# Kernel tuning notes

Hardware: AMD Instinct MI355X
Metric: run time of the kernel (lower is better)

The kernel has to match this reference:

```python
import jax, jax.numpy as jnp
import numpy as np
import math

B, N, C = 2, 2048, 1024
H, HD = 16, 64
COND_SCALE = 0.5
ROPE_THETA = 10000.0


def _layernorm(x, w, b, eps=1e-5):
    mu = jnp.mean(x, axis=-1, keepdims=True)
    var = jnp.mean(jnp.square(x - mu), axis=-1, keepdims=True)
    return (x - mu) * jax.lax.rsqrt(var + eps) * w + b


def _rope_cos_sin(n_pos, dim, dtype):
    # standard 1D RoPE: freqs over half the head dim
    inv = 1.0 / (ROPE_THETA ** (jnp.arange(0, dim, 2, dtype=jnp.float32) / dim))
    ang = jnp.arange(n_pos, dtype=jnp.float32)[:, None] * inv[None, :]  # (n_pos, dim/2)
    cos = jnp.concatenate([jnp.cos(ang), jnp.cos(ang)], axis=-1).astype(dtype)
    sin = jnp.concatenate([jnp.sin(ang), jnp.sin(ang)], axis=-1).astype(dtype)
    return cos, sin


def _apply_rope(x, cos, sin):
    # x: (B,H,N,HD); cos/sin: (N,HD)
    x1, x2 = jnp.split(x, 2, axis=-1)
    rot = jnp.concatenate([-x2, x1], axis=-1)
    return x * cos + rot * sin


def setup_inputs() -> dict:
    key = jax.random.key(0)
    ks = jax.random.split(key, 3)
    s = 1.0 / math.sqrt(C)
    return {
        "x": jax.random.normal(ks[0], (B, N, C), jnp.float32),
        "qkv_w": jax.random.normal(ks[1], (3 * C, C), jnp.float32) * s,
        "qn_w": jnp.ones((HD,), jnp.float32),
        "qn_b": jnp.zeros((HD,), jnp.float32),
        "kn_w": jnp.ones((HD,), jnp.float32),
        "kn_b": jnp.zeros((HD,), jnp.float32),
        "proj_w": jax.random.normal(ks[2], (C, C), jnp.float32) * s,
        "proj_b": jnp.zeros((C,), jnp.float32),
    }


def reference(x, qkv_w, qn_w, qn_b, kn_w, kn_b, proj_w, proj_b):
    b, n, c = x.shape
    n_in = n // 2
    qkv = (x @ qkv_w.T).reshape(b, n, 3, H, HD).transpose(2, 0, 3, 1, 4)
    q, k, v = qkv[0], qkv[1], qkv[2]  # each (B,H,N,HD)
    q = _layernorm(q, qn_w, qn_b)
    k = _layernorm(k, kn_w, kn_b)
    # conditional: rope applied per-half with positions restarting at 0,
    # i.e. cos/sin for positions [0..n_in) tiled over both halves
    cos, sin = _rope_cos_sin(n_in, HD, x.dtype)
    cos = jnp.concatenate([cos, cos], axis=0)  # (N,HD)
    sin = jnp.concatenate([sin, sin], axis=0)
    q = _apply_rope(q, cos, sin)
    k = _apply_rope(k, cos, sin)
    # attn bias: log(conditioning_scale) on cross (input<->cond) blocks
    is_input = jnp.arange(n) < n_in
    cross = is_input[:, None] != is_input[None, :]
    bias = jnp.where(cross, jnp.float32(math.log(COND_SCALE)), 0.0).astype(x.dtype)
    scale = HD ** -0.5
    scores = jnp.einsum("bhqd,bhkd->bhqk", q, k) * scale + bias
    attn = jax.nn.softmax(scores, axis=-1)
    o = jnp.einsum("bhqk,bhkd->bhqd", attn, v)
    o = o.transpose(0, 2, 1, 3).reshape(b, n, c)
    return o @ proj_w.T + proj_b
```

## Files before the change

kernel.cpp:

```cpp
#include <hip/hip_runtime.h>

#define DEVI __device__ __forceinline__

typedef __attribute__((ext_vector_type(8)))  short bh8;
typedef __attribute__((ext_vector_type(4)))  float fx4;
typedef __attribute__((ext_vector_type(16))) float fx16;

DEVI unsigned short f2b(float f){
  unsigned u = __float_as_uint(f);
  u += 0x7FFFu + ((u >> 16) & 1u);
  return (unsigned short)(u >> 16);
}
DEVI float b2f(unsigned short b){ return __uint_as_float(((unsigned)b) << 16); }

DEVI unsigned cvtpk(float a, float b){
  unsigned r;
  asm("v_cvt_pk_bf16_f32 %0, %1, %2" : "=v"(r) : "v"(a), "v"(b));
  return r;
}
DEVI float fexp2(float x){
  float r;
  asm("v_exp_f32 %0, %1" : "=v"(r) : "v"(x));
  return r;
}

typedef __attribute__((address_space(1))) const void gvoid;
typedef __attribute__((address_space(3))) void svoid;
DEVI void gload16(const void* g, void* l){
  __builtin_amdgcn_global_load_lds((gvoid*)g, (svoid*)l, 16, 0, 0);
}

union pfu { unsigned u[4]; bh8 v; };

__global__ __launch_bounds__(256) void cast3_kernel(
    const float* __restrict__ x, const float* __restrict__ w1f, const float* __restrict__ w2f,
    unsigned short* __restrict__ x16, unsigned short* __restrict__ w1, unsigned short* __restrict__ w2)
{
  int i = blockIdx.x * 256 + threadIdx.x;
  const float* src; unsigned short* dst; int off;
  if (i < 1048576)      { src = x;   dst = x16; off = i; }
  else if (i < 1835008) { src = w1f; dst = w1;  off = i - 1048576; }
  else                  { src = w2f; dst = w2;  off = i - 1835008; }
  float4 v = ((const float4*)src)[off];
  short4 r;
  r.x = (short)f2b(v.x); r.y = (short)f2b(v.y);
  r.z = (short)f2b(v.z); r.w = (short)f2b(v.w);
  ((short4*)dst)[off] = r;
}

__global__ __launch_bounds__(256) void rope_table(float* __restrict__ ct, float* __restrict__ st){
  int i = blockIdx.x * 256 + threadIdx.x;
  int pos = i >> 5, j = i & 31;
  float freq = __expf(-(float)j * 0.28782313662425576f);
  float sv, cv; sincosf((float)pos * freq, &sv, &cv);
  ct[i] = cv; st[i] = sv;
}

template<int MODE>
__global__ __launch_bounds__(256) void gemm_bt(
    const unsigned short* __restrict__ A, const unsigned short* __restrict__ B,
    unsigned short* __restrict__ Cb, float* __restrict__ Cf,
    const float* __restrict__ bias, int M, int N, int K)
{
  __shared__ char sm[49152];
  const int t = threadIdx.x, wv = t >> 6, ln = t & 63, lr = ln & 15, lg = ln >> 4;
  const int nbx = gridDim.x, nby = gridDim.y, nwg = nbx * nby;
  const int orig = blockIdx.y * nbx + blockIdx.x;
  const int w = (orig & 7) * (nwg >> 3) + (orig >> 3);
  const int bn = (w / nby) << 7, bm = (w % nby) << 7;
  const int wr = wv >> 1, wc = wv & 1;
  const fx4 fz = {0.f, 0.f, 0.f, 0.f};
  fx4 acc[4][4];
#pragma unroll
  for (int i = 0; i < 4; i++)
#pragma unroll
    for (int j = 0; j < 4; j++) acc[i][j] = fz;
  const int kiters = K >> 5;

#define GSTAGE(dst, k0) do{                                                       \
  _Pragma("unroll")                                                               \
  for (int i_ = 0; i_ < 2; i_++){                                                 \
    int c_ = i_*256 + t;                                                          \
    int row_ = c_ >> 2, col_ = (c_ & 3) << 3;                                     \
    gload16(A + (size_t)(bm + row_)*K + (k0) + col_, (dst) + i_*4096 + wv*1024);  \
    gload16(B + (size_t)(bn + row_)*K + (k0) + col_,                              \
            (dst) + 8192 + i_*4096 + wv*1024);                                    \
  } }while(0)

  char* p0 = sm; char* p1 = sm + 16384; char* p2 = sm + 32768;
  GSTAGE(p0, 0);
  GSTAGE(p1, 32);
  asm volatile("s_waitcnt vmcnt(0)" ::: "memory");
  __builtin_amdgcn_s_barrier();
  __builtin_amdgcn_sched_barrier(0);

  for (int ki = 0; ki < kiters; ++ki){
    if (ki + 2 < kiters) GSTAGE(p2, (ki + 2) << 5);
    bh8 af[4], bf[4];
#pragma unroll
    for (int mi = 0; mi < 4; mi++)
      af[mi] = *(const bh8*)(p0 + (wr*64 + mi*16 + lr)*64 + lg*16);
#pragma unroll
    for (int ni = 0; ni < 4; ni++)
      bf[ni] = *(const bh8*)(p0 + 8192 + (wc*64 + ni*16 + lr)*64 + lg*16);
    __builtin_amdgcn_s_setprio(1);
#pragma unroll
    for (int mi = 0; mi < 4; mi++)
#pragma unroll
      for (int ni = 0; ni < 4; ni++)
        acc[mi][ni] = __builtin_amdgcn_mfma_f32_16x16x32_bf16(af[mi], bf[ni], acc[mi][ni], 0, 0, 0);
    __builtin_amdgcn_s_setprio(0);
    if (ki + 2 < kiters) asm volatile("s_waitcnt vmcnt(4) lgkmcnt(0)" ::: "memory");
    else                 asm volatile("s_waitcnt vmcnt(0) lgkmcnt(0)" ::: "memory");
    __builtin_amdgcn_s_barrier();
    __builtin_amdgcn_sched_barrier(0);
    char* tmp = p0; p0 = p1; p1 = p2; p2 = tmp;
  }
#undef GSTAGE
#pragma unroll
  for (int mi = 0; mi < 4; mi++)
#pragma unroll
    for (int ni = 0; ni < 4; ni++){
      int col = bn + wc*64 + ni*16 + lr;
#pragma unroll
      for (int r = 0; r < 4; r++){
        int row = bm + wr*64 + mi*16 + lg*4 + r;
        float v = acc[mi][ni][r];
        if constexpr (MODE == 1) Cf[(size_t)row * N + col] = v + bias[col];
        else                     Cb[(size_t)row * N + col] = (short)f2b(v);
      }
    }
}

#define QSCALE 0.18033688011112042f
__global__ __launch_bounds__(256) void lnrope_kernel(
    const unsigned short* __restrict__ qkv,
    const float* __restrict__ qw, const float* __restrict__ qb,
    const float* __restrict__ kw, const float* __restrict__ kb,
    const float* __restrict__ ct, const float* __restrict__ st,
    unsigned short* __restrict__ qo, unsigned short* __restrict__ ko,
    unsigned short* __restrict__ vt)
{
  __shared__ short vl[64][66];
  const int t = threadIdx.x, wv = t >> 6, ln = t & 63;
  const int nc = blockIdx.x & 31, h = (blockIdx.x >> 5) & 15, b = blockIdx.x >> 9;
  const int j = ln & 31;
  const float gwq = qw[ln], gbq = qb[ln], gwk = kw[ln], gbk = kb[ln];
  const float sgn = (ln < 32) ? -1.0f : 1.0f;
  const size_t obase0 = ((size_t)(b*16 + h)) * 2048 * 64;
#pragma unroll 1
  for (int it = 0; it < 16; ++it){
    int nl = wv*16 + it;
    int n  = nc*64 + nl;
    size_t base = ((size_t)(b*2048 + n)) * 3072 + h*64 + ln;
    float qv = b2f(qkv[base]);
    float kv = b2f(qkv[base + 1024]);
    float vv = b2f(qkv[base + 2048]);
    float s1 = qv, s2 = qv*qv, s3 = kv, s4 = kv*kv;
#pragma unroll
    for (int off = 32; off; off >>= 1){
      s1 += __shfl_xor(s1, off); s2 += __shfl_xor(s2, off);
      s3 += __shfl_xor(s3, off); s4 += __shfl_xor(s4, off);
    }
    float mq = s1 * (1.f/64.f), mk = s3 * (1.f/64.f);
    float rq = rsqrtf(s2*(1.f/64.f) - mq*mq + 1e-5f);
    float rk = rsqrtf(s4*(1.f/64.f) - mk*mk + 1e-5f);
    float qn = (qv - mq) * rq * gwq + gbq;
    float kn = (kv - mk) * rk * gwk + gbk;
    int pos = n & 1023;
    float cv = ct[pos*32 + j], sv = st[pos*32 + j];
    float qp = __shfl_xor(qn, 32);
    float kp = __shfl_xor(kn, 32);
    size_t ob = obase0 + (size_t)n*64 + ln;
    qo[ob] = f2b((qn*cv + sgn*qp*sv) * QSCALE);
    ko[ob] = f2b(kn*cv + sgn*kp*sv);
    vl[ln][nl] = (short)f2b(vv);
  }
  __syncthreads();
  int d = t >> 2, seg = t & 3;
  size_t vb = (((size_t)(b*16 + h))*64 + d) * 2048 + nc*64 + seg*16;
#pragma unroll
  for (int u = 0; u < 4; ++u){
    short4 pk;
    pk.x = vl[d][seg*16 + u*4 + 0]; pk.y = vl[d][seg*16 + u*4 + 1];
    pk.z = vl[d][seg*16 + u*4 + 2]; pk.w = vl[d][seg*16 + u*4 + 3];
    *(short4*)&vt[vb + u*4] = pk;
  }
}

__global__ __launch_bounds__(512, 4) void attn_kernel(
    const unsigned short* __restrict__ qg, const unsigned short* __restrict__ kg,
    const unsigned short* __restrict__ vg, unsigned short* __restrict__ og)
{
  __shared__ char sm[49152];
  const int t = threadIdx.x, wv = t >> 6, ln = t & 63, lq = ln & 31, hi = ln >> 5;
  const int kvh = wv >> 2;
  const int wq  = wv & 3;
  const int swz = ((blockIdx.x & 7) << 6) | (blockIdx.x >> 3);
  const int bh = swz >> 4, q0 = (swz & 15) << 7;
  const unsigned short* kbase = kg + ((size_t)bh << 17);
  const unsigned short* vbase = vg + ((size_t)bh << 17);
  const size_t qrow = ((size_t)bh << 11) + q0 + wq*32 + lq;
  bh8 qf[4];
#pragma unroll
  for (int s2 = 0; s2 < 4; s2++) qf[s2] = *(const bh8*)&qg[qrow*64 + s2*16 + hi*8];

  fx16 o0, o1;
#pragma unroll
  for (int i = 0; i < 16; i++){ o0[i] = 0.f; o1[i] = 0.f; }
  float l_r = 0.f;
  const bool qfirst = (q0 < 1024);
  const int swsl = lq & 7;

#define STAGE(dst, kt) do{                                                        \
    int row_ = t >> 3, sl_ = (t & 7) ^ (row_ & 7);                                \
    gload16(kbase + (size_t)((kt) + row_)*64 + sl_*8, (dst) + wv*1024);           \
    gload16(vbase + (size_t)row_*2048 + (kt) + sl_*8, (dst) + 8192 + wv*1024);    \
  }while(0)

  char* p0 = sm; char* p1 = sm + 16384; char* p2 = sm + 32768;
  STAGE(p0, 0);
  STAGE(p1, 64);
  asm volatile("s_waitcnt vmcnt(0)" ::: "memory");
  __builtin_amdgcn_s_barrier();
  __builtin_amdgcn_sched_barrier(0);

  for (int tile = 0; tile < 32; ++tile){
    if (tile < 30) STAGE(p2, (tile + 2)*64);
    const char* Kc = p0;
    const char* Vc = p0 + 8192;
    const float bias2 = (qfirst != (tile < 16)) ? -1.0f : 0.0f;
    fx16 sA;
#pragma unroll
    for (int i = 0; i < 16; i++) sA[i] = bias2;
    __builtin_amdgcn_s_setprio(1);
#pragma unroll
    for (int s2 = 0; s2 < 4; s2++){
      const int slot = s2*2 + hi;
      bh8 kf = *(const bh8*)(Kc + (kvh*32 + lq)*128 + ((slot ^ swsl) << 4));
      sA = __builtin_amdgcn_mfma_f32_32x32x16_bf16(kf, qf[s2], sA, 0, 0, 0);
    }
    __builtin_amdgcn_s_setprio(0);
    bh8 vf0[2], vf1[2];
#pragma unroll
    for (int kg2 = 0; kg2 < 2; kg2++){
      const int slot = kvh*4 + kg2*2 + hi;
      vf0[kg2] = *(const bh8*)(Vc + lq*128      + ((slot ^ swsl) << 4));
      vf1[kg2] = *(const bh8*)(Vc + (32+lq)*128 + ((slot ^ swsl) << 4));
    }
    float sum = 0.f;
#pragma unroll
    for (int i = 0; i < 16; i++){
      sA[i] = fexp2(sA[i] - 16.0f);
      sum += sA[i];
    }
    sum += __shfl_xor(sum, 32);
    l_r += sum;
    bh8 pf[2];
#define MKPF(dst, sv, base) do{                                                   \
    unsigned c0 = cvtpk(sv[base+0], sv[base+1]);                                  \
    unsigned c1 = cvtpk(sv[base+2], sv[base+3]);                                  \
    unsigned c2 = cvtpk(sv[base+4], sv[base+5]);                                  \
    unsigned c3 = cvtpk(sv[base+6], sv[base+7]);                                  \
    asm volatile("v_permlane32_swap_b32 %0, %1" : "+v"(c0), "+v"(c2));            \
    asm volatile("v_permlane32_swap_b32 %0, %1" : "+v"(c1), "+v"(c3));            \
    pfu u_; u_.u[0]=c0; u_.u[1]=c1; u_.u[2]=c2; u_.u[3]=c3; dst = u_.v; }while(0)
    MKPF(pf[0], sA, 0); MKPF(pf[1], sA, 8);
#undef MKPF
    __builtin_amdgcn_s_setprio(1);
#pragma unroll
    for (int kg2 = 0; kg2 < 2; kg2++){
      o0 = __builtin_amdgcn_mfma_f32_32x32x16_bf16(vf0[kg2], pf[kg2], o0, 0, 0, 0);
      o1 = __builtin_amdgcn_mfma_f32_32x32x16_bf16(vf1[kg2], pf[kg2], o1, 0, 0, 0);
    }
    __builtin_amdgcn_s_setprio(0);
    if (tile < 30) asm volatile("s_waitcnt vmcnt(2) lgkmcnt(0)" ::: "memory");
    else           asm volatile("s_waitcnt vmcnt(0) lgkmcnt(0)" ::: "memory");
    __builtin_amdgcn_s_barrier();
    __builtin_amdgcn_sched_barrier(0);
    char* tmp = p0; p0 = p1; p1 = p2; p2 = tmp;
  }
#undef STAGE
  float* fbuf = (float*)sm;
  {
    const int base = (wq*64 + ln)*33;
    if (kvh == 1){
#pragma unroll
      for (int i = 0; i < 16; i++){ fbuf[base+i] = o0[i]; fbuf[base+16+i] = o1[i]; }
      fbuf[base+32] = l_r;
    }
  }
  __syncthreads();
  {
    const int base = (wq*64 + ln)*33;
    if (kvh == 0){
#pragma unroll
      for (int i = 0; i < 16; i++){ o0[i] += fbuf[base+i]; o1[i] += fbuf[base+16+i]; }
      l_r += fbuf[base+32];
    }
  }
  __syncthreads();
  if (kvh == 0){
    const float inv = 1.0f / l_r;
    const int ql = wq*32 + lq;
#pragma unroll
    for (int j = 0; j < 8; j++){
      int d0 = ((2*j) & 3) + 8*(j >> 1) + 4*hi;
      unsigned w0 = cvtpk(o0[2*j]*inv, o0[2*j+1]*inv);
      unsigned w1 = cvtpk(o1[2*j]*inv, o1[2*j+1]*inv);
      *(unsigned*)(sm + ql*132 + d0*2)        = w0;
      *(unsigned*)(sm + ql*132 + (32 + d0)*2) = w1;
    }
  }
  __syncthreads();
  if (t < 256){
    const int rw = t >> 1, hf = t & 1;
    const int b = bh >> 4, h = bh & 15;
    unsigned short* dst = og + ((size_t)b*2048 + q0 + rw)*1024 + h*64 + hf*32;
#pragma unroll
    for (int u = 0; u < 8; u++){
      short4 v4 = *(short4*)(sm + rw*132 + hf*64 + u*8);
      *(short4*)(dst + u*4) = v4;
    }
  }
}

extern "C" void kernel_launch(void* const* d_in, const int* in_sizes, int n_in,
                              void* d_out, int out_size, void* d_ws, size_t ws_size,
                              hipStream_t stream)
{
  const float* x      = (const float*)d_in[0];
  const float* qkv_w  = (const float*)d_in[1];
  const float* qn_w   = (const float*)d_in[2];
  const float* qn_b   = (const float*)d_in[3];
  const float* kn_w   = (const float*)d_in[4];
  const float* kn_b   = (const float*)d_in[5];
  const float* proj_w = (const float*)d_in[6];
  const float* proj_b = (const float*)d_in[7];
  float* out = (float*)d_out;

  unsigned short* x16   = (unsigned short*)d_ws;
  unsigned short* w1    = x16   + (size_t)4096*1024;
  unsigned short* w2    = w1    + (size_t)3072*1024;
  unsigned short* qkv16 = w2    + (size_t)1024*1024;
  unsigned short* q16   = qkv16 + (size_t)4096*3072;
  unsigned short* k16   = q16   + (size_t)4194304;
  unsigned short* vt16  = k16   + (size_t)4194304;
  unsigned short* o16   = qkv16;
  float* ct = (float*)x16;
  float* st = ct + 32768;

  cast3_kernel<<<8192, 256, 0, stream>>>(x, qkv_w, proj_w, x16, w1, w2);
  gemm_bt<0><<<dim3(24, 32), 256, 0, stream>>>(x16, w1, qkv16, nullptr, nullptr, 4096, 3072, 1024);
  rope_table<<<128, 256, 0, stream>>>(ct, st);
  lnrope_kernel<<<1024, 256, 0, stream>>>(qkv16, qn_w, qn_b, kn_w, kn_b, ct, st, q16, k16, vt16);
  attn_kernel<<<512, 512, 0, stream>>>(q16, k16, vt16, o16);
  gemm_bt<1><<<dim3(8, 32), 256, 0, stream>>>(o16, w2, nullptr, out, proj_b, 4096, 1024, 1024);
}
```

Before: 138.3 us.

## Add 256x256-tile 4-stage pipelined GEMM for the QKV projection

Replaces the 128x128-tile GEMM for the QKV projection with a new kernel. It uses 256x256 output tiles, 512 threads per block and a 4-deep shared-memory ring of async global-to-LDS loads with explicit vmcnt waits. The larger tiles cut global reloads of A and B and give each wave more MFMA work per LDS read. In exchange, 128KB of LDS limits the kernel to one block per CU, and the grid is only 192 blocks, which may leave compute units idle. The LDS reads are also not swizzled, so bank conflicts may occur.

```diff
diff --git a/kernel.cpp b/kernel.cpp
--- a/kernel.cpp
+++ b/kernel.cpp
@@ -54,6 +54,81 @@
   float freq = __expf(-(float)j * 0.28782313662425576f);
   float sv, cv; sincosf((float)pos * freq, &sv, &cv);
   ct[i] = cv; st[i] = sv;
+}
+
+__global__ __launch_bounds__(512, 2) void gemm256(
+    const unsigned short* __restrict__ A, const unsigned short* __restrict__ B,
+    unsigned short* __restrict__ Cb, int M, int N, int K)
+{
+  __shared__ char sm[131072];
+  const int t = threadIdx.x, wv = t >> 6, ln = t & 63, lr = ln & 15, lg = ln >> 4;
+  const int wr = wv >> 2, wc = wv & 3;
+  const int nwg = gridDim.x * gridDim.y, nby = gridDim.y;
+  const int orig = blockIdx.y * gridDim.x + blockIdx.x;
+  const int w = (orig & 7) * (nwg >> 3) + (orig >> 3);
+  const int bn = (w / nby) << 8, bm = (w % nby) << 8;
+  const fx4 fz = {0.f, 0.f, 0.f, 0.f};
+  fx4 acc[8][4];
+#pragma unroll
+  for (int i = 0; i < 8; i++)
+#pragma unroll
+    for (int j = 0; j < 4; j++) acc[i][j] = fz;
+  const int kiters = K >> 5;
+
+#define GSTAGE(buf, k0) do{                                                       \
+  char* dst_ = sm + ((buf) << 15);                                                \
+  _Pragma("unroll")                                                               \
+  for (int i_ = 0; i_ < 2; i_++){                                                 \
+    int c_ = i_*512 + t;                                                          \
+    int row_ = c_ >> 2, col_ = (c_ & 3) << 3;                                     \
+    gload16(A + (size_t)(bm + row_)*K + (k0) + col_, dst_ + i_*8192 + wv*1024);   \
+    gload16(B + (size_t)(bn + row_)*K + (k0) + col_,                              \
+            dst_ + 16384 + i_*8192 + wv*1024);                                    \
+  } }while(0)
+
+  GSTAGE(0, 0);
+  GSTAGE(1, 32);
+  GSTAGE(2, 64);
+  asm volatile("s_waitcnt vmcnt(0)" ::: "memory");
+  __builtin_amdgcn_s_barrier();
+  __builtin_amdgcn_sched_barrier(0);
+
+  for (int s = 0; s < kiters; ++s){
+    if (s + 3 < kiters) GSTAGE((s + 3) & 3, (s + 3) << 5);
+    const char* Ac = sm + ((s & 3) << 15);
+    const char* Bc = Ac + 16384;
+    bh8 af[8], bf[4];
+#pragma unroll
+    for (int mi = 0; mi < 8; mi++)
+      af[mi] = *(const bh8*)(Ac + (wr*128 + mi*16 + lr)*64 + lg*16);
+#pragma unroll
+    for (int ni = 0; ni < 4; ni++)
+      bf[ni] = *(const bh8*)(Bc + (wc*64 + ni*16 + lr)*64 + lg*16);
+    __builtin_amdgcn_s_setprio(1);
+#pragma unroll
+    for (int mi = 0; mi < 8; mi++)
+#pragma unroll
+      for (int ni = 0; ni < 4; ni++)
+        acc[mi][ni] = __builtin_amdgcn_mfma_f32_16x16x32_bf16(af[mi], bf[ni], acc[mi][ni], 0, 0, 0);
+    __builtin_amdgcn_s_setprio(0);
+    if (s + 3 < kiters)       asm volatile("s_waitcnt vmcnt(8) lgkmcnt(0)" ::: "memory");
+    else if (s + 3 == kiters) asm volatile("s_waitcnt vmcnt(4) lgkmcnt(0)" ::: "memory");
+    else                      asm volatile("s_waitcnt vmcnt(0) lgkmcnt(0)" ::: "memory");
+    __builtin_amdgcn_s_barrier();
+    __builtin_amdgcn_sched_barrier(0);
+  }
+#undef GSTAGE
+#pragma unroll
+  for (int mi = 0; mi < 8; mi++)
+#pragma unroll
+    for (int ni = 0; ni < 4; ni++){
+      int col = bn + wc*64 + ni*16 + lr;
+#pragma unroll
+      for (int r = 0; r < 4; r++){
+        int row = bm + wr*128 + mi*16 + lg*4 + r;
+        Cb[(size_t)row * N + col] = (short)f2b(acc[mi][ni][r]);
+      }
+    }
 }
 
 template<int MODE>
@@ -351,7 +426,7 @@
   float* st = ct + 32768;
 
   cast3_kernel<<<8192, 256, 0, stream>>>(x, qkv_w, proj_w, x16, w1, w2);
-  gemm_bt<0><<<dim3(24, 32), 256, 0, stream>>>(x16, w1, qkv16, nullptr, nullptr, 4096, 3072, 1024);
+  gemm256<<<dim3(12, 16), 512, 0, stream>>>(x16, w1, qkv16, 4096, 3072, 1024);
   rope_table<<<128, 256, 0, stream>>>(ct, st);
   lnrope_kernel<<<1024, 256, 0, stream>>>(qkv16, qn_w, qn_b, kn_w, kn_b, ct, st, q16, k16, vt16);
   attn_kernel<<<512, 512, 0, stream>>>(q16, k16, vt16, o16);
```

New measurement: 139.7 us. No clear change (+1.0%).

## Fuse QK LayerNorm, RoPE and V transpose into QKV GEMM epilogue

Applied to the files above, without the earlier changes.

The QKV projection GEMM now applies per-head LayerNorm and RoPE to the Q and K tiles in registers, and writes V directly in transposed layout. The separate lnrope kernel and the bf16 QKV intermediate buffer are removed. This cuts a full write and re-read of the 4096x3072 intermediate plus one launch. In exchange the GEMM epilogue does more work and issues scattered 2-byte stores for Q and K.

```diff
diff --git a/kernel.cpp b/kernel.cpp
--- a/kernel.cpp
+++ b/kernel.cpp
@@ -56,11 +56,15 @@
   ct[i] = cv; st[i] = sv;
 }
 
-template<int MODE>
-__global__ __launch_bounds__(256) void gemm_bt(
+#define QSCALE 0.18033688011112042f
+
+__global__ __launch_bounds__(256) void gemm_qkv(
     const unsigned short* __restrict__ A, const unsigned short* __restrict__ B,
-    unsigned short* __restrict__ Cb, float* __restrict__ Cf,
-    const float* __restrict__ bias, int M, int N, int K)
+    const float* __restrict__ qnw, const float* __restrict__ qnb,
+    const float* __restrict__ knw, const float* __restrict__ knb,
+    const float* __restrict__ ct, const float* __restrict__ st,
+    unsigned short* __restrict__ qo, unsigned short* __restrict__ ko,
+    unsigned short* __restrict__ vt, int N, int K)
 {
   __shared__ char sm[49152];
   const int t = threadIdx.x, wv = t >> 6, ln = t & 63, lr = ln & 15, lg = ln >> 4;
@@ -117,6 +121,126 @@
     char* tmp = p0; p0 = p1; p1 = p2; p2 = tmp;
   }
 #undef GSTAGE
+
+  const int col0 = bn + wc*64;
+  const int which = col0 >> 10;
+  const int h = (col0 >> 6) & 15;
+  const int rowbase = bm + wr*64;
+  if (which == 2){
+#pragma unroll
+    for (int mi = 0; mi < 4; mi++)
+#pragma unroll
+      for (int ni = 0; ni < 4; ni++){
+        int row = rowbase + mi*16 + lg*4;
+        int b = row >> 11, n = row & 2047;
+        size_t vb = (((size_t)(b*16 + h))*64 + ni*16 + lr)*2048 + n;
+        short4 pk;
+        pk.x = (short)f2b(acc[mi][ni][0]);
+        pk.y = (short)f2b(acc[mi][ni][1]);
+        pk.z = (short)f2b(acc[mi][ni][2]);
+        pk.w = (short)f2b(acc[mi][ni][3]);
+        *(short4*)&vt[vb] = pk;
+      }
+  } else {
+    const float* gw = which ? knw : qnw;
+    const float* gb = which ? knb : qnb;
+    const float w0 = gw[lr], w1_ = gw[16+lr], w2_ = gw[32+lr], w3 = gw[48+lr];
+    const float b0 = gb[lr], b1_ = gb[16+lr], b2_ = gb[32+lr], b3 = gb[48+lr];
+    const float qs = which ? 1.0f : QSCALE;
+    unsigned short* dst = which ? ko : qo;
+#pragma unroll
+    for (int mi = 0; mi < 4; mi++)
+#pragma unroll
+      for (int r = 0; r < 4; r++){
+        float x0 = acc[mi][0][r], x1 = acc[mi][1][r];
+        float x2 = acc[mi][2][r], x3 = acc[mi][3][r];
+        float s  = (x0 + x1) + (x2 + x3);
+        float q2 = (x0*x0 + x1*x1) + (x2*x2 + x3*x3);
+#pragma unroll
+        for (int off = 1; off < 16; off <<= 1){
+          s  += __shfl_xor(s,  off);
+          q2 += __shfl_xor(q2, off);
+        }
+        float mean = s * (1.f/64.f);
+        float rstd = rsqrtf(q2*(1.f/64.f) - mean*mean + 1e-5f);
+        float y0 = (x0-mean)*rstd*w0 + b0, y1 = (x1-mean)*rstd*w1_ + b1_;
+        float y2 = (x2-mean)*rstd*w2_ + b2_, y3 = (x3-mean)*rstd*w3 + b3;
+        int row = rowbase + mi*16 + lg*4 + r;
+        int b = row >> 11, n = row & 2047, pos = row & 1023;
+        float c0 = ct[pos*32 + lr],      s0 = st[pos*32 + lr];
+        float c1 = ct[pos*32 + 16 + lr], s1 = st[pos*32 + 16 + lr];
+        float o0 = (y0*c0 - y2*s0) * qs;
+        float o1 = (y1*c1 - y3*s1) * qs;
+        float o2 = (y2*c0 + y0*s0) * qs;
+        float o3 = (y3*c1 + y1*s1) * qs;
+        size_t ob = (((size_t)(b*16 + h))*2048 + n)*64;
+        dst[ob + lr]      = f2b(o0);
+        dst[ob + 16 + lr] = f2b(o1);
+        dst[ob + 32 + lr] = f2b(o2);
+        dst[ob + 48 + lr] = f2b(o3);
+      }
+  }
+}
+
+__global__ __launch_bounds__(256) void gemm_bt(
+    const unsigned short* __restrict__ A, const unsigned short* __restrict__ B,
+    float* __restrict__ Cf, const float* __restrict__ bias, int M, int N, int K)
+{
+  __shared__ char sm[49152];
+  const int t = threadIdx.x, wv = t >> 6, ln = t & 63, lr = ln & 15, lg = ln >> 4;
+  const int nbx = gridDim.x, nby = gridDim.y, nwg = nbx * nby;
+  const int orig = blockIdx.y * nbx + blockIdx.x;
+  const int w = (orig & 7) * (nwg >> 3) + (orig >> 3);
+  const int bn = (w / nby) << 7, bm = (w % nby) << 7;
+  const int wr = wv >> 1, wc = wv & 1;
+  const fx4 fz = {0.f, 0.f, 0.f, 0.f};
+  fx4 acc[4][4];
+#pragma unroll
+  for (int i = 0; i < 4; i++)
+#pragma unroll
+    for (int j = 0; j < 4; j++) acc[i][j] = fz;
+  const int kiters = K >> 5;
+
+#define GSTAGE(dst, k0) do{                                                       \
+  _Pragma("unroll")                                                               \
+  for (int i_ = 0; i_ < 2; i_++){                                                 \
+    int c_ = i_*256 + t;                                                          \
+    int row_ = c_ >> 2, col_ = (c_ & 3) << 3;                                     \
+    gload16(A + (size_t)(bm + row_)*K + (k0) + col_, (dst) + i_*4096 + wv*1024);  \
+    gload16(B + (size_t)(bn + row_)*K + (k0) + col_,                              \
+            (dst) + 8192 + i_*4096 + wv*1024);                                    \
+  } }while(0)
+
+  char* p0 = sm; char* p1 = sm + 16384; char* p2 = sm + 32768;
+  GSTAGE(p0, 0);
+  GSTAGE(p1, 32);
+  asm volatile("s_waitcnt vmcnt(0)" ::: "memory");
+  __builtin_amdgcn_s_barrier();
+  __builtin_amdgcn_sched_barrier(0);
+
+  for (int ki = 0; ki < kiters; ++ki){
+    if (ki + 2 < kiters) GSTAGE(p2, (ki + 2) << 5);
+    bh8 af[4], bf[4];
+#pragma unroll
+    for (int mi = 0; mi < 4; mi++)
+      af[mi] = *(const bh8*)(p0 + (wr*64 + mi*16 + lr)*64 + lg*16);
+#pragma unroll
+    for (int ni = 0; ni < 4; ni++)
+      bf[ni] = *(const bh8*)(p0 + 8192 + (wc*64 + ni*16 + lr)*64 + lg*16);
+    __builtin_amdgcn_s_setprio(1);
+#pragma unroll
+    for (int mi = 0; mi < 4; mi++)
+#pragma unroll
+      for (int ni = 0; ni < 4; ni++)
+        acc[mi][ni] = __builtin_amdgcn_mfma_f32_16x16x32_bf16(af[mi], bf[ni], acc[mi][ni], 0, 0, 0);
+    __builtin_amdgcn_s_setprio(0);
+    if (ki + 2 < kiters) asm volatile("s_waitcnt vmcnt(4) lgkmcnt(0)" ::: "memory");
+    else                 asm volatile("s_waitcnt vmcnt(0) lgkmcnt(0)" ::: "memory");
+    __builtin_amdgcn_s_barrier();
+    __builtin_amdgcn_sched_barrier(0);
+    char* tmp = p0; p0 = p1; p1 = p2; p2 = tmp;
+  }
+#undef GSTAGE
 #pragma unroll
   for (int mi = 0; mi < 4; mi++)
 #pragma unroll
@@ -125,67 +249,9 @@
 #pragma unroll
       for (int r = 0; r < 4; r++){
         int row = bm + wr*64 + mi*16 + lg*4 + r;
-        float v = acc[mi][ni][r];
-        if constexpr (MODE == 1) Cf[(size_t)row * N + col] = v + bias[col];
-        else                     Cb[(size_t)row * N + col] = (short)f2b(v);
+        Cf[(size_t)row * N + col] = acc[mi][ni][r] + bias[col];
       }
     }
-}
-
-#define QSCALE 0.18033688011112042f
-__global__ __launch_bounds__(256) void lnrope_kernel(
-    const unsigned short* __restrict__ qkv,
-    const float* __restrict__ qw, const float* __restrict__ qb,
-    const float* __restrict__ kw, const float* __restrict__ kb,
-    const float* __restrict__ ct, const float* __restrict__ st,
-    unsigned short* __restrict__ qo, unsigned short* __restrict__ ko,
-    unsigned short* __restrict__ vt)
-{
-  __shared__ short vl[64][66];
-  const int t = threadIdx.x, wv = t >> 6, ln = t & 63;
-  const int nc = blockIdx.x & 31, h = (blockIdx.x >> 5) & 15, b = blockIdx.x >> 9;
-  const int j = ln & 31;
-  const float gwq = qw[ln], gbq = qb[ln], gwk = kw[ln], gbk = kb[ln];
-  const float sgn = (ln < 32) ? -1.0f : 1.0f;
-  const size_t obase0 = ((size_t)(b*16 + h)) * 2048 * 64;
-#pragma unroll 1
-  for (int it = 0; it < 16; ++it){
-    int nl = wv*16 + it;
-    int n  = nc*64 + nl;
-    size_t base = ((size_t)(b*2048 + n)) * 3072 + h*64 + ln;
-    float qv = b2f(qkv[base]);
-    float kv = b2f(qkv[base + 1024]);
-    float vv = b2f(qkv[base + 2048]);
-    float s1 = qv, s2 = qv*qv, s3 = kv, s4 = kv*kv;
-#pragma unroll
-    for (int off = 32; off; off >>= 1){
-      s1 += __shfl_xor(s1, off); s2 += __shfl_xor(s2, off);
-      s3 += __shfl_xor(s3, off); s4 += __shfl_xor(s4, off);
-    }
-    float mq = s1 * (1.f/64.f), mk = s3 * (1.f/64.f);
-    float rq = rsqrtf(s2*(1.f/64.f) - mq*mq + 1e-5f);
-    float rk = rsqrtf(s4*(1.f/64.f) - mk*mk + 1e-5f);
-    float qn = (qv - mq) * rq * gwq + gbq;
-    float kn = (kv - mk) * rk * gwk + gbk;
-    int pos = n & 1023;
-    float cv = ct[pos*32 + j], sv = st[pos*32 + j];
-    float qp = __shfl_xor(qn, 32);
-    float kp = __shfl_xor(kn, 32);
-    size_t ob = obase0 + (size_t)n*64 + ln;
-    qo[ob] = f2b((qn*cv + sgn*qp*sv) * QSCALE);
-    ko[ob] = f2b(kn*cv + sgn*kp*sv);
-    vl[ln][nl] = (short)f2b(vv);
-  }
-  __syncthreads();
-  int d = t >> 2, seg = t & 3;
-  size_t vb = (((size_t)(b*16 + h))*64 + d) * 2048 + nc*64 + seg*16;
-#pragma unroll
-  for (int u = 0; u < 4; ++u){
-    short4 pk;
-    pk.x = vl[d][seg*16 + u*4 + 0]; pk.y = vl[d][seg*16 + u*4 + 1];
-    pk.z = vl[d][seg*16 + u*4 + 2]; pk.w = vl[d][seg*16 + u*4 + 3];
-    *(short4*)&vt[vb + u*4] = pk;
-  }
 }
 
 __global__ __launch_bounds__(512, 4) void attn_kernel(
@@ -342,18 +408,18 @@
   unsigned short* x16   = (unsigned short*)d_ws;
   unsigned short* w1    = x16   + (size_t)4096*1024;
   unsigned short* w2    = w1    + (size_t)3072*1024;
-  unsigned short* qkv16 = w2    + (size_t)1024*1024;
-  unsigned short* q16   = qkv16 + (size_t)4096*3072;
+  unsigned short* scr   = w2    + (size_t)1024*1024;
+  unsigned short* q16   = scr   + (size_t)4096*3072;
   unsigned short* k16   = q16   + (size_t)4194304;
   unsigned short* vt16  = k16   + (size_t)4194304;
-  unsigned short* o16   = qkv16;
-  float* ct = (float*)x16;
+  float* ct = (float*)scr;
   float* st = ct + 32768;
+  unsigned short* o16   = scr + 262144;
 
   cast3_kernel<<<8192, 256, 0, stream>>>(x, qkv_w, proj_w, x16, w1, w2);
-  gemm_bt<0><<<dim3(24, 32), 256, 0, stream>>>(x16, w1, qkv16, nullptr, nullptr, 4096, 3072, 1024);
   rope_table<<<128, 256, 0, stream>>>(ct, st);
-  lnrope_kernel<<<1024, 256, 0, stream>>>(qkv16, qn_w, qn_b, kn_w, kn_b, ct, st, q16, k16, vt16);
+  gemm_qkv<<<dim3(24, 32), 256, 0, stream>>>(x16, w1, qn_w, qn_b, kn_w, kn_b,
+                                             ct, st, q16, k16, vt16, 3072, 1024);
   attn_kernel<<<512, 512, 0, stream>>>(q16, k16, vt16, o16);
-  gemm_bt<1><<<dim3(8, 32), 256, 0, stream>>>(o16, w2, nullptr, out, proj_b, 4096, 1024, 1024);
-}
+  gemm_bt<<<dim3(8, 32), 256, 0, stream>>>(o16, w2, out, proj_b, 4096, 1024, 1024);
+}
```

After: 124.2 us. -10.2%, faster.
